# Performance work log

Hardware: AMD Instinct MI355X
Metric: run time of the kernel (lower is better)

The kernel has to match this reference:

```python
import jax, jax.numpy as jnp
import numpy as np
from jax import lax

B, C, H, W = 64, 256, 32, 32
EPS = 1e-5


def setup_inputs() -> dict:
    key = jax.random.key(0)
    ks = jax.random.split(key, 11)
    c = C
    return {
        "x": jax.random.normal(ks[0], (B, C, H, W), jnp.float32),
        "bn1_gamma": jax.random.uniform(ks[1], (c,), jnp.float32, 0.5, 1.5),
        "bn1_beta": 0.1 * jax.random.normal(ks[2], (c,), jnp.float32),
        "bn1_mean": 0.1 * jax.random.normal(ks[3], (c,), jnp.float32),
        "bn1_var": jax.random.uniform(ks[4], (c,), jnp.float32, 0.5, 1.5),
        "w1": 0.05 * jax.random.normal(ks[5], (c, c, 3, 3), jnp.float32),
        "bn2_gamma": jax.random.uniform(ks[6], (c,), jnp.float32, 0.5, 1.5),
        "bn2_beta": 0.1 * jax.random.normal(ks[7], (c,), jnp.float32),
        "bn2_mean": 0.1 * jax.random.normal(ks[8], (c,), jnp.float32),
        "bn2_var": jax.random.uniform(ks[9], (c,), jnp.float32, 0.5, 1.5),
        "w2": 0.05 * jax.random.normal(ks[10], (c, c, 3, 3), jnp.float32),
    }


def _bn(x, gamma, beta, mean, var):
    # eval-mode BatchNorm2d over channel axis of NCHW
    inv = gamma * lax.rsqrt(var + EPS)
    return x * inv[None, :, None, None] + (beta - mean * inv)[None, :, None, None]


def _binarize(x):
    # TBN binary activations {-1,+1}, straight-through in bwd
    s = jnp.where(x >= 0, 1.0, -1.0).astype(x.dtype)
    return x + lax.stop_gradient(s - x)


def _ternarize(w):
    # TBN ternary weights alpha*{-1,0,+1}; delta = 0.7*mean|W|
    aw = jnp.abs(w)
    delta = 0.7 * jnp.mean(aw)
    mask = (aw > delta).astype(w.dtype)
    alpha = jnp.sum(aw * mask) / jnp.maximum(jnp.sum(mask), 1.0)
    wq = alpha * jnp.sign(w) * mask
    return w + lax.stop_gradient(wq - w)


def _tbn_conv3x3(x, w, stride):
    return lax.conv_general_dilated(
        _binarize(x), _ternarize(w),
        window_strides=(stride, stride), padding=[(1, 1), (1, 1)],
        dimension_numbers=("NCHW", "OIHW", "NCHW"))


def reference(x, bn1_gamma, bn1_beta, bn1_mean, bn1_var, w1,
              bn2_gamma, bn2_beta, bn2_mean, bn2_var, w2):
    identity = x
    h = _tbn_conv3x3(_bn(x, bn1_gamma, bn1_beta, bn1_mean, bn1_var), w1, 1)
    h = _tbn_conv3x3(_bn(h, bn2_gamma, bn2_beta, bn2_mean, bn2_var), w2, 1)
    return identity + h  # ShortCut downsample
```

## Files before the change

### kernel.cpp

```cpp
#include <hip/hip_runtime.h>
#include <stdint.h>


#define EPS 1e-5f

typedef int i32x4 __attribute__((ext_vector_type(4)));

__device__ __forceinline__ void gload16(const void* g, void* l) {
  __builtin_amdgcn_global_load_lds(
      (const __attribute__((address_space(1))) void*)g,
      (__attribute__((address_space(3))) void*)l, 16, 0, 0);
}

__global__ __launch_bounds__(256) void wsum_kernel(const float* __restrict__ w,
                                                   float* __restrict__ partial) {
  __shared__ float red[256];
  const int t = threadIdx.x;
  const int b = blockIdx.x;
  float s = 0.f;
#pragma unroll
  for (int i = 0; i < 32; ++i) s += fabsf(w[b * 256 + t + i * 18432]);
  red[t] = s;
  __syncthreads();
  for (int o = 128; o > 0; o >>= 1) {
    if (t < o) red[t] += red[t + o];
    __syncthreads();
  }
  if (t == 0) partial[b] = red[0];
}

__global__ void delta_kernel(const float* __restrict__ p1, const float* __restrict__ p2,
                             float* __restrict__ delta) {
  const int t = threadIdx.x;
  if (t < 2) {
    const float* p = (t == 0) ? p1 : p2;
    double s = 0.0;
    for (int i = 0; i < 72; ++i) s += (double)p[i];
    delta[t] = 0.7f * (float)(s * (1.0 / 589824.0));
  }
}

__global__ __launch_bounds__(256) void quant_kernel(const float* __restrict__ w,
                                                    const float* __restrict__ delta2, const int didx,
                                                    int8_t* __restrict__ wq,
                                                    float* __restrict__ psum,
                                                    float* __restrict__ pcnt) {
  __shared__ float rs[256];
  __shared__ float rc[256];
  const int t = threadIdx.x;
  const int idx = blockIdx.x * 256 + t;
  const float d = delta2[didx];
  const float v = w[idx];
  const float av = fabsf(v);
  const bool m = av > d;
  const int co = idx / 2304;
  const int rem = idx - co * 2304;
  const int ci = rem / 9;
  const int tap = rem - ci * 9;
  const int panel = (ci >> 6) * 9 + tap;
  const int cil = ci & 63;
  const int slot = cil >> 4;
  const int b = cil & 15;
  wq[panel * 16384 + (co >> 6) * 4096 + slot * 1024 + (co & 63) * 16 + b] =
      m ? (v > 0.f ? (int8_t)1 : (int8_t)-1) : (int8_t)0;
  rs[t] = m ? av : 0.f;
  rc[t] = m ? 1.f : 0.f;
  __syncthreads();
  for (int o = 128; o > 0; o >>= 1) {
    if (t < o) { rs[t] += rs[t + o]; rc[t] += rc[t + o]; }
    __syncthreads();
  }
  if (t == 0) { psum[blockIdx.x] = rs[0]; pcnt[blockIdx.x] = rc[0]; }
}

__global__ __launch_bounds__(256) void alpha_kernel(const float* __restrict__ ps1, const float* __restrict__ pc1,
                                                    const float* __restrict__ ps2, const float* __restrict__ pc2,
                                                    const float* __restrict__ g2, const float* __restrict__ b2,
                                                    const float* __restrict__ m2, const float* __restrict__ v2,
                                                    float* __restrict__ alphas,
                                                    float* __restrict__ inv2o, float* __restrict__ add2o) {
  __shared__ float rs[256];
  __shared__ float rc[256];
  const int t = threadIdx.x;
  float s1 = 0.f, c1 = 0.f, s2 = 0.f, c2 = 0.f;
#pragma unroll
  for (int i = 0; i < 9; ++i) {
    s1 += ps1[t + (i << 8)]; c1 += pc1[t + (i << 8)];
    s2 += ps2[t + (i << 8)]; c2 += pc2[t + (i << 8)];
  }
  rs[t] = s1; rc[t] = c1;
  __syncthreads();
  for (int o = 128; o > 0; o >>= 1) {
    if (t < o) { rs[t] += rs[t + o]; rc[t] += rc[t + o]; }
    __syncthreads();
  }
  if (t == 0) alphas[0] = rs[0] / fmaxf(rc[0], 1.f);
  __syncthreads();
  rs[t] = s2; rc[t] = c2;
  __syncthreads();
  for (int o = 128; o > 0; o >>= 1) {
    if (t < o) { rs[t] += rs[t + o]; rc[t] += rc[t + o]; }
    __syncthreads();
  }
  if (t == 0) alphas[1] = rs[0] / fmaxf(rc[0], 1.f);
  const float inv = g2[t] * rsqrtf(v2[t] + EPS);
  inv2o[t] = inv;
  add2o[t] = b2[t] - m2[t] * inv;
}

__global__ __launch_bounds__(256) void bn_bin_kernel(const float* __restrict__ x,
                                                     const float* __restrict__ g1,
                                                     const float* __restrict__ b1,
                                                     const float* __restrict__ m1,
                                                     const float* __restrict__ v1,
                                                     int8_t* __restrict__ a1) {
  __shared__ int8_t lds[64 * 40];
  const int t = threadIdx.x;
  const int p0 = blockIdx.x << 6;
  const int c0 = blockIdx.y << 5;
  const int n = blockIdx.z;
  const int pl = t & 63;
  const int cl0 = t >> 6;
#pragma unroll
  for (int i = 0; i < 8; ++i) {
    const int cl = cl0 + (i << 2);
    const int c = c0 + cl;
    const float inv = g1[c] * rsqrtf(v1[c] + EPS);
    const float ad = b1[c] - m1[c] * inv;
    const float val = x[(((n << 8) + c) << 10) + p0 + pl];
    const float tt = fmaf(val, inv, ad);
    lds[pl * 40 + cl] = (tt >= 0.f) ? (int8_t)1 : (int8_t)-1;
  }
  __syncthreads();
  const int pl2 = t >> 2;
  const int s2 = (t & 3) << 3;
  const uint2 o = *(const uint2*)&lds[pl2 * 40 + s2];
  *(uint2*)&a1[(((n << 10) + p0 + pl2) << 8) + c0 + s2] = o;
}

template <int EPI>
__global__ __launch_bounds__(256) void conv3x3_tbn(
    const int8_t* __restrict__ act,
    const int8_t* __restrict__ wq,
    const float* __restrict__ alphas, const int aidx,
    const float* __restrict__ inv2, const float* __restrict__ add2,
    const float* __restrict__ xres,
    int8_t* __restrict__ aout, float* __restrict__ fout) {
  __shared__ int8_t ldsA[4 * 336 * 16];
  __shared__ int8_t ldsB[9 * 4 * 64 * 16];

  const int tid = threadIdx.x;
  const int bid = blockIdx.x;
  const int L = (bid & 7) * 128 + (bid >> 3);
  const int mb = L >> 2;
  const int nb = L & 3;
  const int n = mb >> 2;
  const int y0 = (mb & 3) << 3;
  const int l = tid & 63;
  const int wid = tid >> 6;
  const int wm = wid >> 1;
  const int wn = wid & 1;
  const int q = l >> 4;
  const int r = l & 15;

  int srcA[5], dstA[5];
#pragma unroll
  for (int i = 0; i < 5; ++i) {
    const int idx = tid + (i << 8);
    const int asl = idx / 320;
    const int apx = idx - asl * 320;
    int ys = y0 - 1 + (apx >> 5);
    ys = ys < 0 ? 0 : (ys > 31 ? 31 : ys);
    srcA[i] = (((n << 10) + (ys << 5) + (apx & 31)) << 8) + (asl << 4);
    dstA[i] = asl * 5376 + (apx << 4);
  }
  if (tid < 4) *(i32x4*)(ldsA + tid * 5376 + 320 * 16) = (i32x4){0, 0, 0, 0};

  int ylocal[8], xcol[8];
#pragma unroll
  for (int mi = 0; mi < 8; ++mi) {
    const int p = wm * 128 + mi * 16 + r;
    ylocal[mi] = p >> 5;
    xcol[mi] = p & 31;
  }
  int bAddr[2];
#pragma unroll
  for (int ni = 0; ni < 2; ++ni)
    bAddr[ni] = (q << 10) + ((wn * 32 + ni * 16 + r) << 4);

  i32x4 acc[8][2];
#pragma unroll
  for (int mi = 0; mi < 8; ++mi)
#pragma unroll
    for (int ni = 0; ni < 2; ++ni) acc[mi][ni] = (i32x4){0, 0, 0, 0};

#pragma unroll
  for (int i = 0; i < 5; ++i) gload16(act + srcA[i], ldsA + dstA[i]);
#pragma unroll
  for (int i = 0; i < 9; ++i)
    gload16(wq + i * 16384 + (nb << 12) + (tid << 4),
            ldsB + (i << 12) + (tid << 4));
  __syncthreads();

  for (int chunk = 0; chunk < 4; ++chunk) {
#pragma unroll
    for (int tap = 0; tap < 9; ++tap) {
      const int ky = tap / 3, kx = tap % 3;
      int aAddr[8];
#pragma unroll
      for (int mi = 0; mi < 8; ++mi) {
        const int xs = xcol[mi] + kx - 1;
        const int ys = y0 + ylocal[mi] + ky - 1;
        const bool valid = ((unsigned)xs < 32u) && ((unsigned)ys < 32u);
        const int apix = valid ? (((ylocal[mi] + ky) << 5) + (xs & 31)) : 320;
        aAddr[mi] = q * 5376 + (apix << 4);
      }
      i32x4 bf[2];
#pragma unroll
      for (int ni = 0; ni < 2; ++ni)
        bf[ni] = *(const i32x4*)(ldsB + (tap << 12) + bAddr[ni]);
      __builtin_amdgcn_s_setprio(1);
#pragma unroll
      for (int mi = 0; mi < 8; ++mi) {
        const i32x4 af = *(const i32x4*)(ldsA + aAddr[mi]);
#pragma unroll
        for (int ni = 0; ni < 2; ++ni)
          acc[mi][ni] = __builtin_amdgcn_mfma_i32_16x16x64_i8(af, bf[ni], acc[mi][ni], 0, 0, 0);
      }
      __builtin_amdgcn_s_setprio(0);
    }
    if (chunk < 3) {
      __syncthreads();
#pragma unroll
      for (int i = 0; i < 5; ++i)
        gload16(act + srcA[i] + ((chunk + 1) << 6), ldsA + dstA[i]);
#pragma unroll
      for (int i = 0; i < 9; ++i)
        gload16(wq + ((chunk + 1) * 9 + i) * 16384 + (nb << 12) + (tid << 4),
                ldsB + (i << 12) + (tid << 4));
      __syncthreads();
    }
  }

  const float alpha = alphas[aidx];
  if constexpr (EPI == 0) {
#pragma unroll
    for (int ni = 0; ni < 2; ++ni) {
      const int co = nb * 64 + wn * 32 + ni * 16 + r;
      const float inv = inv2[co];
      const float ad = add2[co];
#pragma unroll
      for (int mi = 0; mi < 8; ++mi) {
        const int prow0 = mb * 256 + wm * 128 + mi * 16 + (q << 2);
#pragma unroll
        for (int j = 0; j < 4; ++j) {
          const float h = alpha * (float)acc[mi][ni][j];
          const float tt = fmaf(h, inv, ad);
          aout[(prow0 + j) * 256 + co] = (tt >= 0.f) ? (int8_t)1 : (int8_t)-1;
        }
      }
    }
  } else {
#pragma unroll
    for (int ni = 0; ni < 2; ++ni) {
      const int co = nb * 64 + wn * 32 + ni * 16 + r;
#pragma unroll
      for (int mi = 0; mi < 8; ++mi) {
        const int pimg = ((mb & 3) << 8) + wm * 128 + mi * 16 + (q << 2);
        const int off = (((n << 8) + co) << 10) + pimg;
        const float4 xv = *(const float4*)(xres + off);
        float4 o;
        o.x = xv.x + alpha * (float)acc[mi][ni][0];
        o.y = xv.y + alpha * (float)acc[mi][ni][1];
        o.z = xv.z + alpha * (float)acc[mi][ni][2];
        o.w = xv.w + alpha * (float)acc[mi][ni][3];
        *(float4*)(fout + off) = o;
      }
    }
  }
}

extern "C" void kernel_launch(void* const* d_in, const int* in_sizes, int n_in,
                              void* d_out, int out_size, void* d_ws, size_t ws_size,
                              hipStream_t stream) {
  const float* x  = (const float*)d_in[0];
  const float* g1 = (const float*)d_in[1];
  const float* b1 = (const float*)d_in[2];
  const float* m1 = (const float*)d_in[3];
  const float* v1 = (const float*)d_in[4];
  const float* w1 = (const float*)d_in[5];
  const float* g2 = (const float*)d_in[6];
  const float* b2 = (const float*)d_in[7];
  const float* m2 = (const float*)d_in[8];
  const float* v2 = (const float*)d_in[9];
  const float* w2 = (const float*)d_in[10];
  float* out = (float*)d_out;

  char* ws = (char*)d_ws;
  int8_t* a1  = (int8_t*)(ws);
  int8_t* a2  = (int8_t*)(ws + 16777216);
  int8_t* wq1 = (int8_t*)(ws + 33554432);
  int8_t* wq2 = (int8_t*)(ws + 33554432 + 589824);
  float* fs = (float*)(ws + 33554432 + 1179648);
  float* pd1    = fs;
  float* pd2    = fs + 128;
  float* deltas = fs + 256;
  float* alphas = fs + 260;
  float* ps1    = fs + 512;
  float* pc1    = fs + 512 + 2304;
  float* ps2    = fs + 512 + 4608;
  float* pc2    = fs + 512 + 6912;
  float* inv2   = fs + 512 + 9216;
  float* add2   = fs + 512 + 9472;

  hipLaunchKernelGGL(wsum_kernel, dim3(72), dim3(256), 0, stream, w1, pd1);
  hipLaunchKernelGGL(wsum_kernel, dim3(72), dim3(256), 0, stream, w2, pd2);
  hipLaunchKernelGGL(delta_kernel, dim3(1), dim3(64), 0, stream, pd1, pd2, deltas);
  hipLaunchKernelGGL(quant_kernel, dim3(2304), dim3(256), 0, stream, w1, deltas, 0, wq1, ps1, pc1);
  hipLaunchKernelGGL(quant_kernel, dim3(2304), dim3(256), 0, stream, w2, deltas, 1, wq2, ps2, pc2);
  hipLaunchKernelGGL(alpha_kernel, dim3(1), dim3(256), 0, stream,
                     ps1, pc1, ps2, pc2, g2, b2, m2, v2, alphas, inv2, add2);
  hipLaunchKernelGGL(bn_bin_kernel, dim3(16, 8, 64), dim3(256), 0, stream, x, g1, b1, m1, v1, a1);
  hipLaunchKernelGGL((conv3x3_tbn<0>), dim3(1024), dim3(256), 0, stream,
                     a1, wq1, alphas, 0, inv2, add2, (const float*)nullptr,
                     a2, (float*)nullptr);
  hipLaunchKernelGGL((conv3x3_tbn<1>), dim3(1024), dim3(256), 0, stream,
                     a2, wq2, alphas, 1, (const float*)nullptr, (const float*)nullptr, x,
                     (int8_t*)nullptr, out);
  (void)in_sizes; (void)n_in; (void)out_size; (void)ws_size;
}
```

Before: 131.9 us.

## Switch conv to 32x32x32 int8 MFMA with 32-channel output tiles

Each conv block now computes 256 pixels by 32 output channels instead of 64, using 32x32x32 int8 MFMA in place of 16x16x64, and the grid doubles to 2048 blocks. The weight layout is regrouped per 32-channel group so each block loads one contiguous panel, LDS use shrinks, and launch bounds ask for 4 blocks per CU. The aim is more occupancy and fewer LDS fragment reads per MFMA. In exchange every activation tile is loaded twice as often across blocks, and the epilogue's per-byte int8 stores follow a different access pattern.

```diff
diff --git a/kernel.cpp b/kernel.cpp
--- a/kernel.cpp
+++ b/kernel.cpp
@@ -4,7 +4,8 @@
 
 #define EPS 1e-5f
 
-typedef int i32x4 __attribute__((ext_vector_type(4)));
+typedef int i32x4  __attribute__((ext_vector_type(4)));
+typedef int i32x16 __attribute__((ext_vector_type(16)));
 
 __device__ __forceinline__ void gload16(const void* g, void* l) {
   __builtin_amdgcn_global_load_lds(
@@ -57,11 +58,8 @@
   const int rem = idx - co * 2304;
   const int ci = rem / 9;
   const int tap = rem - ci * 9;
-  const int panel = (ci >> 6) * 9 + tap;
-  const int cil = ci & 63;
-  const int slot = cil >> 4;
-  const int b = cil & 15;
-  wq[panel * 16384 + (co >> 6) * 4096 + slot * 1024 + (co & 63) * 16 + b] =
+  wq[(co >> 5) * 73728 + (ci >> 6) * 18432 + tap * 2048 +
+     (((ci & 63) >> 4) << 9) + ((co & 31) << 4) + (ci & 15)] =
       m ? (v > 0.f ? (int8_t)1 : (int8_t)-1) : (int8_t)0;
   rs[t] = m ? av : 0.f;
   rc[t] = m ? 1.f : 0.f;
@@ -139,29 +137,27 @@
 }
 
 template <int EPI>
-__global__ __launch_bounds__(256) void conv3x3_tbn(
+__global__ __launch_bounds__(256, 4) void conv3x3_tbn(
     const int8_t* __restrict__ act,
     const int8_t* __restrict__ wq,
     const float* __restrict__ alphas, const int aidx,
     const float* __restrict__ inv2, const float* __restrict__ add2,
     const float* __restrict__ xres,
     int8_t* __restrict__ aout, float* __restrict__ fout) {
-  __shared__ int8_t ldsA[4 * 336 * 16];
-  __shared__ int8_t ldsB[9 * 4 * 64 * 16];
+  __shared__ int8_t ldsA[4 * 321 * 16];
+  __shared__ int8_t ldsB[9 * 4 * 32 * 16];
 
   const int tid = threadIdx.x;
   const int bid = blockIdx.x;
-  const int L = (bid & 7) * 128 + (bid >> 3);
-  const int mb = L >> 2;
-  const int nb = L & 3;
+  const int L = (bid & 7) * 256 + (bid >> 3);
+  const int mb = L >> 3;
+  const int nb = L & 7;
   const int n = mb >> 2;
   const int y0 = (mb & 3) << 3;
   const int l = tid & 63;
   const int wid = tid >> 6;
-  const int wm = wid >> 1;
-  const int wn = wid & 1;
-  const int q = l >> 4;
-  const int r = l & 15;
+  const int lx = l & 31;
+  const int lh = l >> 5;
 
   int srcA[5], dstA[5];
 #pragma unroll
@@ -172,108 +168,97 @@
     int ys = y0 - 1 + (apx >> 5);
     ys = ys < 0 ? 0 : (ys > 31 ? 31 : ys);
     srcA[i] = (((n << 10) + (ys << 5) + (apx & 31)) << 8) + (asl << 4);
-    dstA[i] = asl * 5376 + (apx << 4);
-  }
-  if (tid < 4) *(i32x4*)(ldsA + tid * 5376 + 320 * 16) = (i32x4){0, 0, 0, 0};
-
-  int ylocal[8], xcol[8];
-#pragma unroll
-  for (int mi = 0; mi < 8; ++mi) {
-    const int p = wm * 128 + mi * 16 + r;
-    ylocal[mi] = p >> 5;
-    xcol[mi] = p & 31;
-  }
-  int bAddr[2];
-#pragma unroll
-  for (int ni = 0; ni < 2; ++ni)
-    bAddr[ni] = (q << 10) + ((wn * 32 + ni * 16 + r) << 4);
-
-  i32x4 acc[8][2];
-#pragma unroll
-  for (int mi = 0; mi < 8; ++mi)
-#pragma unroll
-    for (int ni = 0; ni < 2; ++ni) acc[mi][ni] = (i32x4){0, 0, 0, 0};
+    dstA[i] = asl * 5136 + (apx << 4);
+  }
+  if (tid < 4) *(i32x4*)(ldsA + tid * 5136 + 5120) = (i32x4){0, 0, 0, 0};
+
+  i32x16 acc[2];
+  acc[0] = (i32x16)(0);
+  acc[1] = (i32x16)(0);
+
+  const int8_t* wbase = wq + nb * 73728;
 
 #pragma unroll
   for (int i = 0; i < 5; ++i) gload16(act + srcA[i], ldsA + dstA[i]);
 #pragma unroll
-  for (int i = 0; i < 9; ++i)
-    gload16(wq + i * 16384 + (nb << 12) + (tid << 4),
-            ldsB + (i << 12) + (tid << 4));
+  for (int i = 0; i < 4; ++i)
+    gload16(wbase + ((tid + (i << 8)) << 4), ldsB + ((tid + (i << 8)) << 4));
+  if (tid < 128) gload16(wbase + ((tid + 1024) << 4), ldsB + ((tid + 1024) << 4));
   __syncthreads();
 
   for (int chunk = 0; chunk < 4; ++chunk) {
+    __builtin_amdgcn_s_setprio(1);
 #pragma unroll
     for (int tap = 0; tap < 9; ++tap) {
       const int ky = tap / 3, kx = tap % 3;
-      int aAddr[8];
-#pragma unroll
-      for (int mi = 0; mi < 8; ++mi) {
-        const int xs = xcol[mi] + kx - 1;
-        const int ys = y0 + ylocal[mi] + ky - 1;
-        const bool valid = ((unsigned)xs < 32u) && ((unsigned)ys < 32u);
-        const int apix = valid ? (((ylocal[mi] + ky) << 5) + (xs & 31)) : 320;
-        aAddr[mi] = q * 5376 + (apix << 4);
+      const int xs = lx + kx - 1;
+      const bool xok = (unsigned)xs < 32u;
+      int apix[2];
+#pragma unroll
+      for (int mt = 0; mt < 2; ++mt) {
+        const int yr = (wid << 1) + mt + ky;
+        const bool ok = xok && ((unsigned)(y0 - 1 + yr) < 32u);
+        apix[mt] = ok ? (yr << 5) + xs : 320;
       }
-      i32x4 bf[2];
-#pragma unroll
-      for (int ni = 0; ni < 2; ++ni)
-        bf[ni] = *(const i32x4*)(ldsB + (tap << 12) + bAddr[ni]);
-      __builtin_amdgcn_s_setprio(1);
-#pragma unroll
-      for (int mi = 0; mi < 8; ++mi) {
-        const i32x4 af = *(const i32x4*)(ldsA + aAddr[mi]);
-#pragma unroll
-        for (int ni = 0; ni < 2; ++ni)
-          acc[mi][ni] = __builtin_amdgcn_mfma_i32_16x16x64_i8(af, bf[ni], acc[mi][ni], 0, 0, 0);
+      i32x4 bfr[2], afr[2][2];
+#pragma unroll
+      for (int kh = 0; kh < 2; ++kh) {
+        const int sl = lh + (kh << 1);
+        bfr[kh] = *(const i32x4*)(ldsB + (tap << 11) + (sl << 9) + (lx << 4));
+#pragma unroll
+        for (int mt = 0; mt < 2; ++mt)
+          afr[mt][kh] = *(const i32x4*)(ldsA + sl * 5136 + (apix[mt] << 4));
       }
-      __builtin_amdgcn_s_setprio(0);
+#pragma unroll
+      for (int mt = 0; mt < 2; ++mt)
+#pragma unroll
+        for (int kh = 0; kh < 2; ++kh)
+          acc[mt] = __builtin_amdgcn_mfma_i32_32x32x32_i8(afr[mt][kh], bfr[kh], acc[mt], 0, 0, 0);
     }
+    __builtin_amdgcn_s_setprio(0);
     if (chunk < 3) {
       __syncthreads();
 #pragma unroll
       for (int i = 0; i < 5; ++i)
         gload16(act + srcA[i] + ((chunk + 1) << 6), ldsA + dstA[i]);
-#pragma unroll
-      for (int i = 0; i < 9; ++i)
-        gload16(wq + ((chunk + 1) * 9 + i) * 16384 + (nb << 12) + (tid << 4),
-                ldsB + (i << 12) + (tid << 4));
+      const int8_t* wch = wbase + (chunk + 1) * 18432;
+#pragma unroll
+      for (int i = 0; i < 4; ++i)
+        gload16(wch + ((tid + (i << 8)) << 4), ldsB + ((tid + (i << 8)) << 4));
+      if (tid < 128) gload16(wch + ((tid + 1024) << 4), ldsB + ((tid + 1024) << 4));
       __syncthreads();
     }
   }
 
   const float alpha = alphas[aidx];
+  const int co = (nb << 5) + lx;
   if constexpr (EPI == 0) {
-#pragma unroll
-    for (int ni = 0; ni < 2; ++ni) {
-      const int co = nb * 64 + wn * 32 + ni * 16 + r;
-      const float inv = inv2[co];
-      const float ad = add2[co];
-#pragma unroll
-      for (int mi = 0; mi < 8; ++mi) {
-        const int prow0 = mb * 256 + wm * 128 + mi * 16 + (q << 2);
-#pragma unroll
-        for (int j = 0; j < 4; ++j) {
-          const float h = alpha * (float)acc[mi][ni][j];
-          const float tt = fmaf(h, inv, ad);
-          aout[(prow0 + j) * 256 + co] = (tt >= 0.f) ? (int8_t)1 : (int8_t)-1;
-        }
+    const float inv = inv2[co];
+    const float ad = add2[co];
+#pragma unroll
+    for (int mt = 0; mt < 2; ++mt) {
+      const int pixbase = (mb << 8) + (((wid << 1) + mt) << 5) + (lh << 2);
+#pragma unroll
+      for (int rg = 0; rg < 16; ++rg) {
+        const int pix = pixbase + (rg & 3) + ((rg >> 2) << 3);
+        const float h = alpha * (float)acc[mt][rg];
+        const float tt = fmaf(h, inv, ad);
+        aout[(pix << 8) + co] = (tt >= 0.f) ? (int8_t)1 : (int8_t)-1;
       }
     }
   } else {
 #pragma unroll
-    for (int ni = 0; ni < 2; ++ni) {
-      const int co = nb * 64 + wn * 32 + ni * 16 + r;
-#pragma unroll
-      for (int mi = 0; mi < 8; ++mi) {
-        const int pimg = ((mb & 3) << 8) + wm * 128 + mi * 16 + (q << 2);
-        const int off = (((n << 8) + co) << 10) + pimg;
+    for (int mt = 0; mt < 2; ++mt) {
+      const int pimg0 = ((mb & 3) << 8) + (((wid << 1) + mt) << 5) + (lh << 2);
+#pragma unroll
+      for (int qd = 0; qd < 4; ++qd) {
+        const int off = (((n << 8) + co) << 10) + pimg0 + (qd << 3);
         const float4 xv = *(const float4*)(xres + off);
         float4 o;
-        o.x = xv.x + alpha * (float)acc[mi][ni][0];
-        o.y = xv.y + alpha * (float)acc[mi][ni][1];
-        o.z = xv.z + alpha * (float)acc[mi][ni][2];
-        o.w = xv.w + alpha * (float)acc[mi][ni][3];
+        o.x = xv.x + alpha * (float)acc[mt][qd * 4 + 0];
+        o.y = xv.y + alpha * (float)acc[mt][qd * 4 + 1];
+        o.z = xv.z + alpha * (float)acc[mt][qd * 4 + 2];
+        o.w = xv.w + alpha * (float)acc[mt][qd * 4 + 3];
         *(float4*)(fout + off) = o;
       }
     }
@@ -321,10 +306,10 @@
   hipLaunchKernelGGL(alpha_kernel, dim3(1), dim3(256), 0, stream,
                      ps1, pc1, ps2, pc2, g2, b2, m2, v2, alphas, inv2, add2);
   hipLaunchKernelGGL(bn_bin_kernel, dim3(16, 8, 64), dim3(256), 0, stream, x, g1, b1, m1, v1, a1);
-  hipLaunchKernelGGL((conv3x3_tbn<0>), dim3(1024), dim3(256), 0, stream,
+  hipLaunchKernelGGL((conv3x3_tbn<0>), dim3(2048), dim3(256), 0, stream,
                      a1, wq1, alphas, 0, inv2, add2, (const float*)nullptr,
                      a2, (float*)nullptr);
-  hipLaunchKernelGGL((conv3x3_tbn<1>), dim3(1024), dim3(256), 0, stream,
+  hipLaunchKernelGGL((conv3x3_tbn<1>), dim3(2048), dim3(256), 0, stream,
                      a2, wq2, alphas, 1, (const float*)nullptr, (const float*)nullptr, x,
                      (int8_t*)nullptr, out);
   (void)in_sizes; (void)n_in; (void)out_size; (void)ws_size;
```

New measurement: 135.7 us. 1.03x slower.
